# Kernel tuning notes

Hardware: AMD Instinct MI355X
Metric: run time of the kernel (lower is better)

The kernel has to match this reference:

```python
import jax, jax.numpy as jnp
import numpy as np

N = 50000   # nodes
E = 600000  # edges
D = 128     # in_size
H = 128     # hid_size
O = 10      # out_size


def setup_inputs() -> dict:
    key = jax.random.key(0)
    ks = jax.random.split(key, 11)
    features = jax.random.normal(ks[0], (N, D), dtype=jnp.float32)
    src = jax.random.randint(ks[1], (E,), 0, N, dtype=jnp.int32)
    dst = jax.random.randint(ks[2], (E,), 0, N, dtype=jnp.int32)
    s = 1.0 / np.sqrt(D)
    # 4 GraphConv layers: D->H, H->H, H->H, H->O (DGL GraphConv: weight + bias)
    W0 = jax.random.normal(ks[3], (D, H), jnp.float32) * s
    b0 = jnp.zeros((H,), jnp.float32)
    W1 = jax.random.normal(ks[4], (H, H), jnp.float32) * s
    b1 = jnp.zeros((H,), jnp.float32)
    W2 = jax.random.normal(ks[5], (H, H), jnp.float32) * s
    b2 = jnp.zeros((H,), jnp.float32)
    W3 = jax.random.normal(ks[6], (H, O), jnp.float32) * s
    b3 = jnp.zeros((O,), jnp.float32)
    return {"features": features, "src": src, "dst": dst,
            "W0": W0, "b0": b0, "W1": W1, "b1": b1,
            "W2": W2, "b2": b2, "W3": W3, "b3": b3}


def reference(features, src, dst, W0, b0, W1, b1, W2, b2, W3, b3):
    # DGL GraphConv with norm='both':
    #   h' = relu( D_in^{-1/2} A D_out^{-1/2} h W + b )
    # degrees clamped to >= 1; dropout is inference-mode identity.
    ones = jnp.ones((E,), features.dtype)
    out_deg = jax.ops.segment_sum(ones, src, num_segments=N)
    in_deg = jax.ops.segment_sum(ones, dst, num_segments=N)
    out_inv = jax.lax.rsqrt(jnp.maximum(out_deg, 1.0))[:, None]  # [N,1]
    in_inv = jax.lax.rsqrt(jnp.maximum(in_deg, 1.0))[:, None]    # [N,1]

    h = features
    layers = [(W0, b0, True), (W1, b1, True), (W2, b2, True), (W3, b3, False)]
    for W, b, act in layers:
        hs = h * out_inv                                   # src-side norm
        agg = jax.ops.segment_sum(hs[src], dst, num_segments=N)  # SpMM (copy_u + sum)
        h = (agg * in_inv) @ W + b                         # dst-side norm + linear
        if act:
            h = jax.nn.relu(h)
    return h
```

## Files before the change

### kernel.cpp

```cpp
#include <hip/hip_runtime.h>

#define NNODES 50000
#define NEDGES 600000
#define DH 128
#define SCAN_THREADS 512
#define SCAN_ELEMS 2048
#define SCAN_BLOCKS ((NNODES + SCAN_ELEMS - 1) / SCAN_ELEMS)
#define WCONV_BLOCKS ((3 * DH * DH) / 256)
#define NSLICES 32
#define NCHUNKS 8
#define CHUNK (NNODES / NCHUNKS)
#define ESLICE (NEDGES / NSLICES)
#define CNT_THREADS 1024

typedef __attribute__((ext_vector_type(4))) float f32x4;
typedef __attribute__((ext_vector_type(4))) _Float16 half4;
typedef __attribute__((ext_vector_type(8))) _Float16 half8;

__global__ __launch_bounds__(CNT_THREADS) void count_chunked(
        const int* __restrict__ src, const int* __restrict__ dst,
        int* __restrict__ partIn, int* __restrict__ partOut) {
    __shared__ int hin[CHUNK];
    __shared__ int hout[CHUNK];
    int slice = blockIdx.x >> 3;
    int chunk = blockIdx.x & 7;
    int cbase = chunk * CHUNK;
    int t = threadIdx.x;
    for (int i = t; i < CHUNK; i += CNT_THREADS) { hin[i] = 0; hout[i] = 0; }
    __syncthreads();
    int e0 = slice * ESLICE;
    int e1 = e0 + ESLICE;
    for (int e = e0 + t; e < e1; e += CNT_THREADS) {
        int d = dst[e];
        unsigned dd = (unsigned)(d - cbase);
        if (dd < CHUNK) atomicAdd(&hin[dd], 1);
        int s = src[e];
        unsigned ss = (unsigned)(s - cbase);
        if (ss < CHUNK) atomicAdd(&hout[ss], 1);
    }
    __syncthreads();
    int* pi = partIn  + slice * NNODES + cbase;
    int* po = partOut + slice * NNODES + cbase;
    for (int i = t; i < CHUNK; i += CNT_THREADS) { pi[i] = hin[i]; po[i] = hout[i]; }
}

__global__ void reduce_counts(const int* __restrict__ partIn, const int* __restrict__ partOut,
                              int* __restrict__ cnt_in, int* __restrict__ cnt_out, int N) {
    int n = blockIdx.x * blockDim.x + threadIdx.x;
    if (n >= N) return;
    int ti = 0, to = 0;
#pragma unroll
    for (int s = 0; s < NSLICES; ++s) {
        ti += partIn[s * NNODES + n];
        to += partOut[s * NNODES + n];
    }
    cnt_in[n] = ti;
    cnt_out[n] = to;
}

__global__ __launch_bounds__(SCAN_THREADS) void scan_sums(
        const int* __restrict__ counts, int* __restrict__ bsums, int N) {
    __shared__ int red[SCAN_THREADS / 64];
    int b = blockIdx.x, t = threadIdx.x;
    int base = b * SCAN_ELEMS + t * 4;
    int s = 0;
    if (base + 3 < N) {
        int4 v = *(const int4*)(counts + base);
        s = v.x + v.y + v.z + v.w;
    } else {
        for (int j = 0; j < 4; ++j) if (base + j < N) s += counts[base + j];
    }
#pragma unroll
    for (int off = 32; off > 0; off >>= 1) s += __shfl_down(s, off);
    if ((t & 63) == 0) red[t >> 6] = s;
    __syncthreads();
    if (t == 0) {
        int tot = 0;
#pragma unroll
        for (int w = 0; w < SCAN_THREADS / 64; ++w) tot += red[w];
        bsums[b] = tot;
    }
}

__global__ __launch_bounds__(SCAN_THREADS) void scan_final(
        const int* __restrict__ counts, const int* __restrict__ bsums,
        const int* __restrict__ cnt_out, int* __restrict__ off,
        int* __restrict__ cursor, float* __restrict__ out_inv,
        float* __restrict__ in_inv, int N, int nb) {
    __shared__ int lds[SCAN_THREADS];
    __shared__ int base_s;
    int b = blockIdx.x, t = threadIdx.x;
    if (t == 0) {
        int acc = 0;
        for (int i = 0; i < b; ++i) acc += bsums[i];
        base_s = acc;
    }
    int i0 = b * SCAN_ELEMS + t * 4;
    int v[4]; int s = 0;
#pragma unroll
    for (int j = 0; j < 4; ++j) {
        int idx = i0 + j;
        v[j] = (idx < N) ? counts[idx] : 0;
        s += v[j];
    }
    lds[t] = s;
    __syncthreads();
    for (int d = 1; d < SCAN_THREADS; d <<= 1) {
        int x = lds[t];
        int y = (t >= d) ? lds[t - d] : 0;
        __syncthreads();
        lds[t] = x + y;
        __syncthreads();
    }
    int excl = (t == 0) ? 0 : lds[t - 1];
    int run = base_s + excl;
#pragma unroll
    for (int j = 0; j < 4; ++j) {
        int idx = i0 + j;
        if (idx < N) {
            off[idx]    = run;
            cursor[idx] = run;
            in_inv[idx]  = rsqrtf(fmaxf((float)v[j], 1.0f));
            out_inv[idx] = rsqrtf(fmaxf((float)cnt_out[idx], 1.0f));
        }
        run += v[j];
    }
    if (b == nb - 1 && t == SCAN_THREADS - 1) off[N] = run;
}

__global__ void scatter_kernel(const int* __restrict__ src, const int* __restrict__ dst,
                               int* __restrict__ cursor, int* __restrict__ csr_src, int E) {
    int i = blockIdx.x * blockDim.x + threadIdx.x;
    if (i < E) {
        int pos = atomicAdd(&cursor[dst[i]], 1);
        csr_src[pos] = src[i];
    }
}

__global__ void prep_kernel(const float* __restrict__ W0, const float* __restrict__ W1,
                            const float* __restrict__ W2,
                            _Float16* __restrict__ WThi, _Float16* __restrict__ WTlo,
                            const float* __restrict__ fin, const float* __restrict__ out_inv,
                            _Float16* __restrict__ fout, int n4) {
    if (blockIdx.x < WCONV_BLOCKS) {
        int t = blockIdx.x * blockDim.x + threadIdx.x;
        int L = t >> 14;
        int idx = t & (DH * DH - 1);
        int n = idx >> 7;
        int k = idx & 127;
        const float* W = (L == 0) ? W0 : ((L == 1) ? W1 : W2);
        float w = W[k * DH + n];
        _Float16 hi = (_Float16)w;
        _Float16 lo = (_Float16)(w - (float)hi);
        WThi[t] = hi;
        WTlo[t] = lo;
    } else {
        int i = (blockIdx.x - WCONV_BLOCKS) * blockDim.x + threadIdx.x;
        if (i < n4) {
            float sc = out_inv[i >> 5];
            float4 v = ((const float4*)fin)[i];
            half4 h = {(_Float16)(v.x * sc), (_Float16)(v.y * sc),
                       (_Float16)(v.z * sc), (_Float16)(v.w * sc)};
            ((half4*)fout)[i] = h;
        }
    }
}

__global__ __launch_bounds__(256) void spmm_csr(
        const _Float16* __restrict__ h, const int* __restrict__ row_off,
        const int* __restrict__ csr_src,
        const float* __restrict__ in_inv, _Float16* __restrict__ X, int N) {
    int gw   = (blockIdx.x * blockDim.x + threadIdx.x) >> 6;
    int lane = threadIdx.x & 63;
    int half = lane >> 5;
    int l5   = lane & 31;
    int row  = gw * 2 + half;
    if (row >= N) return;
    int start = row_off[row], end = row_off[row + 1];
    float4 acc0 = make_float4(0.f, 0.f, 0.f, 0.f);
    float4 acc1 = make_float4(0.f, 0.f, 0.f, 0.f);
    int e = start;
    for (; e + 8 <= end; e += 8) {
        int s0 = csr_src[e];
        int s1 = csr_src[e + 1];
        int s2 = csr_src[e + 2];
        int s3 = csr_src[e + 3];
        int s4 = csr_src[e + 4];
        int s5 = csr_src[e + 5];
        int s6 = csr_src[e + 6];
        int s7 = csr_src[e + 7];
        half4 v0 = ((const half4*)(h + (size_t)s0 * DH))[l5];
        half4 v1 = ((const half4*)(h + (size_t)s1 * DH))[l5];
        half4 v2 = ((const half4*)(h + (size_t)s2 * DH))[l5];
        half4 v3 = ((const half4*)(h + (size_t)s3 * DH))[l5];
        half4 v4 = ((const half4*)(h + (size_t)s4 * DH))[l5];
        half4 v5 = ((const half4*)(h + (size_t)s5 * DH))[l5];
        half4 v6 = ((const half4*)(h + (size_t)s6 * DH))[l5];
        half4 v7 = ((const half4*)(h + (size_t)s7 * DH))[l5];
        acc0.x += (float)v0.x; acc0.y += (float)v0.y; acc0.z += (float)v0.z; acc0.w += (float)v0.w;
        acc1.x += (float)v1.x; acc1.y += (float)v1.y; acc1.z += (float)v1.z; acc1.w += (float)v1.w;
        acc0.x += (float)v2.x; acc0.y += (float)v2.y; acc0.z += (float)v2.z; acc0.w += (float)v2.w;
        acc1.x += (float)v3.x; acc1.y += (float)v3.y; acc1.z += (float)v3.z; acc1.w += (float)v3.w;
        acc0.x += (float)v4.x; acc0.y += (float)v4.y; acc0.z += (float)v4.z; acc0.w += (float)v4.w;
        acc1.x += (float)v5.x; acc1.y += (float)v5.y; acc1.z += (float)v5.z; acc1.w += (float)v5.w;
        acc0.x += (float)v6.x; acc0.y += (float)v6.y; acc0.z += (float)v6.z; acc0.w += (float)v6.w;
        acc1.x += (float)v7.x; acc1.y += (float)v7.y; acc1.z += (float)v7.z; acc1.w += (float)v7.w;
    }
    for (; e + 2 <= end; e += 2) {
        int s0 = csr_src[e];
        int s1 = csr_src[e + 1];
        half4 v0 = ((const half4*)(h + (size_t)s0 * DH))[l5];
        half4 v1 = ((const half4*)(h + (size_t)s1 * DH))[l5];
        acc0.x += (float)v0.x; acc0.y += (float)v0.y; acc0.z += (float)v0.z; acc0.w += (float)v0.w;
        acc1.x += (float)v1.x; acc1.y += (float)v1.y; acc1.z += (float)v1.z; acc1.w += (float)v1.w;
    }
    if (e < end) {
        int s0 = csr_src[e];
        half4 v0 = ((const half4*)(h + (size_t)s0 * DH))[l5];
        acc0.x += (float)v0.x; acc0.y += (float)v0.y; acc0.z += (float)v0.z; acc0.w += (float)v0.w;
    }
    float ii = in_inv[row];
    half4 o;
    o.x = (_Float16)((acc0.x + acc1.x) * ii);
    o.y = (_Float16)((acc0.y + acc1.y) * ii);
    o.z = (_Float16)((acc0.z + acc1.z) * ii);
    o.w = (_Float16)((acc0.w + acc1.w) * ii);
    ((half4*)(X + (size_t)row * DH))[l5] = o;
}

template<int RELU>
__global__ __launch_bounds__(256, 2) void gemm_mfma(
        const _Float16* __restrict__ X,
        const _Float16* __restrict__ WThi, const _Float16* __restrict__ WTlo,
        const float* __restrict__ bias, const float* __restrict__ out_inv,
        _Float16* __restrict__ Y, int Mtiles) {
    int lane  = threadIdx.x & 63;
    int gwave = (blockIdx.x * blockDim.x + threadIdx.x) >> 6;
    int nwav  = (gridDim.x * blockDim.x) >> 6;
    int nhalf = gwave & 1;
    int wstart  = gwave >> 1;
    int wstride = nwav >> 1;

    int r  = lane & 15;
    int kq = lane >> 4;

    half8 B[2][4][4];
#pragma unroll
    for (int nt = 0; nt < 4; ++nt) {
        int n = 64 * nhalf + 16 * nt + r;
#pragma unroll
        for (int kf = 0; kf < 4; ++kf) {
            B[0][nt][kf] = *(const half8*)(WThi + n * DH + 32 * kf + 8 * kq);
            B[1][nt][kf] = *(const half8*)(WTlo + n * DH + 32 * kf + 8 * kq);
        }
    }
    float bs[4];
#pragma unroll
    for (int nt = 0; nt < 4; ++nt) bs[nt] = bias[64 * nhalf + 16 * nt + r];

    for (int mt = wstart; mt < Mtiles; mt += wstride) {
        int m0 = mt * 16;
        const _Float16* xp = X + (size_t)(m0 + r) * DH + 8 * kq;
        half8 A[4];
#pragma unroll
        for (int kf = 0; kf < 4; ++kf)
            A[kf] = *(const half8*)(xp + 32 * kf);
        f32x4 acc[4];
#pragma unroll
        for (int nt = 0; nt < 4; ++nt)
            acc[nt] = (f32x4){bs[nt], bs[nt], bs[nt], bs[nt]};
#pragma unroll
        for (int kf = 0; kf < 4; ++kf) {
#pragma unroll
            for (int nt = 0; nt < 4; ++nt) {
                acc[nt] = __builtin_amdgcn_mfma_f32_16x16x32_f16(A[kf], B[0][nt][kf], acc[nt], 0, 0, 0);
                acc[nt] = __builtin_amdgcn_mfma_f32_16x16x32_f16(A[kf], B[1][nt][kf], acc[nt], 0, 0, 0);
            }
        }
        float sc[4];
#pragma unroll
        for (int j = 0; j < 4; ++j) sc[j] = out_inv[m0 + 4 * kq + j];
#pragma unroll
        for (int nt = 0; nt < 4; ++nt) {
            int n = 64 * nhalf + 16 * nt + r;
            _Float16* yp = Y + (size_t)(m0 + 4 * kq) * DH + n;
#pragma unroll
            for (int j = 0; j < 4; ++j) {
                float v = acc[nt][j];
                if (RELU) v = fmaxf(v, 0.f);
                yp[(size_t)j * DH] = (_Float16)(v * sc[j]);
            }
        }
    }
}

__global__ __launch_bounds__(256) void proj_out(
        const _Float16* __restrict__ X,
        const float* __restrict__ W, float* __restrict__ Z, int N) {
    __shared__ float Wl[DH * 10];
    for (int i = threadIdx.x; i < DH * 10; i += blockDim.x) Wl[i] = W[i];
    __syncthreads();

    int row = blockIdx.x * blockDim.x + threadIdx.x;
    if (row >= N) return;

    float acc[10];
#pragma unroll
    for (int o = 0; o < 10; ++o) acc[o] = 0.f;

    const half8* xp = (const half8*)(X + (size_t)row * DH);
#pragma unroll
    for (int q = 0; q < 16; ++q) {
        half8 v = xp[q];
#pragma unroll
        for (int j = 0; j < 8; ++j) {
            float x = (float)v[j];
            const float* wp = Wl + (q * 8 + j) * 10;
#pragma unroll
            for (int o = 0; o < 10; ++o)
                acc[o] += x * wp[o];
        }
    }
    float* zp = Z + (size_t)row * 10;
#pragma unroll
    for (int o = 0; o < 10; ++o) zp[o] = acc[o];
}

__global__ void agg10(const float* __restrict__ Z, const int* __restrict__ row_off,
                      const int* __restrict__ csr_src, const float* __restrict__ in_inv,
                      const float* __restrict__ b, float* __restrict__ out, int N) {
    int r = blockIdx.x * blockDim.x + threadIdx.x;
    if (r >= N) return;
    float2 acc[5] = {};
    int start = row_off[r], end = row_off[r + 1];
    for (int e = start; e < end; ++e) {
        int s = csr_src[e];
        const float2* zp = (const float2*)(Z + (size_t)s * 10);
#pragma unroll
        for (int o = 0; o < 5; ++o) {
            float2 z = zp[o];
            acc[o].x += z.x; acc[o].y += z.y;
        }
    }
    float ii = in_inv[r];
#pragma unroll
    for (int o = 0; o < 5; ++o) {
        out[(size_t)r * 10 + 2 * o]     = acc[o].x * ii + b[2 * o];
        out[(size_t)r * 10 + 2 * o + 1] = acc[o].y * ii + b[2 * o + 1];
    }
}

extern "C" void kernel_launch(void* const* d_in, const int* in_sizes, int n_in,
                              void* d_out, int out_size, void* d_ws, size_t ws_size,
                              hipStream_t stream) {
    const float* features = (const float*)d_in[0];
    const int*   src      = (const int*)d_in[1];
    const int*   dst      = (const int*)d_in[2];
    const float* W0 = (const float*)d_in[3];
    const float* b0 = (const float*)d_in[4];
    const float* W1 = (const float*)d_in[5];
    const float* b1 = (const float*)d_in[6];
    const float* W2 = (const float*)d_in[7];
    const float* b2 = (const float*)d_in[8];
    const float* W3 = (const float*)d_in[9];
    const float* b3 = (const float*)d_in[10];
    float* out = (float*)d_out;

    char* ws = (char*)d_ws;
    int*   cnt_out = (int*)ws;
    int*   cnt_in  = cnt_out + NNODES;
    int*   cursor  = cnt_in + NNODES;
    int*   row_off = cursor + NNODES;
    int*   bsums   = row_off + NNODES + 1;
    float* out_inv = (float*)(bsums + SCAN_BLOCKS);
    float* in_inv  = out_inv + NNODES;
    int*   csr_src = (int*)(in_inv + NNODES);
    size_t metaInts = (size_t)(6 * NNODES + 1 + SCAN_BLOCKS) + NEDGES;
    size_t off = ((metaInts * 4 + 255) / 256) * 256;
    _Float16* WThi = (_Float16*)(ws + off);  off += 3 * DH * DH * sizeof(_Float16);
    _Float16* WTlo = (_Float16*)(ws + off);  off += 3 * DH * DH * sizeof(_Float16);
    off = ((off + 255) / 256) * 256;
    _Float16* X16 = (_Float16*)(ws + off); off += (size_t)NNODES * DH * sizeof(_Float16);
    _Float16* Y16 = (_Float16*)(ws + off); off += (size_t)NNODES * DH * sizeof(_Float16);
    _Float16* F16 = (_Float16*)(ws + off); off += (size_t)NNODES * DH * sizeof(_Float16);
    float*  Z   = (float*)X16;
    int* partIn  = (int*)X16;
    int* partOut = (int*)Y16;

    const int n4 = NNODES * DH / 4;

    count_chunked<<<NSLICES * NCHUNKS, CNT_THREADS, 0, stream>>>(src, dst, partIn, partOut);
    reduce_counts<<<(NNODES + 255) / 256, 256, 0, stream>>>(partIn, partOut, cnt_in, cnt_out, NNODES);
    scan_sums<<<SCAN_BLOCKS, SCAN_THREADS, 0, stream>>>(cnt_in, bsums, NNODES);
    scan_final<<<SCAN_BLOCKS, SCAN_THREADS, 0, stream>>>(cnt_in, bsums, cnt_out, row_off,
                                                         cursor, out_inv, in_inv, NNODES, SCAN_BLOCKS);
    scatter_kernel<<<(NEDGES + 255) / 256, 256, 0, stream>>>(src, dst, cursor, csr_src, NEDGES);
    prep_kernel<<<WCONV_BLOCKS + (n4 + 255) / 256, 256, 0, stream>>>(W0, W1, W2, WThi, WTlo,
                                                                     features, out_inv, F16, n4);

    const int spmm_blocks = (NNODES / 2 + 3) / 4;
    const int Mtiles = NNODES / 16;
    const int gemm_blocks = 512;

    spmm_csr<<<spmm_blocks, 256, 0, stream>>>(F16, row_off, csr_src, in_inv, X16, NNODES);
    gemm_mfma<1><<<gemm_blocks, 256, 0, stream>>>(X16, WThi, WTlo, b0, out_inv, Y16, Mtiles);
    spmm_csr<<<spmm_blocks, 256, 0, stream>>>(Y16, row_off, csr_src, in_inv, X16, NNODES);
    gemm_mfma<1><<<gemm_blocks, 256, 0, stream>>>(X16, WThi + DH * DH, WTlo + DH * DH, b1, out_inv, Y16, Mtiles);
    spmm_csr<<<spmm_blocks, 256, 0, stream>>>(Y16, row_off, csr_src, in_inv, X16, NNODES);
    gemm_mfma<1><<<gemm_blocks, 256, 0, stream>>>(X16, WThi + 2 * DH * DH, WTlo + 2 * DH * DH, b2, out_inv, Y16, Mtiles);
    proj_out<<<(NNODES + 255) / 256, 256, 0, stream>>>(Y16, W3, Z, NNODES);
    agg10<<<(NNODES + 255) / 256, 256, 0, stream>>>(Z, row_off, csr_src, in_inv, b3, out, NNODES);
}
```

Measured before the change: 229.7 us.

## Fuse SpMM aggregation and MFMA GEMM into one per-tile layer kernel

Replaces the separate spmm_csr and gemm_mfma kernels with a single fused_layer kernel. Each 512-thread block aggregates 16 destination rows into an LDS tile, then eight waves each compute one 16-column slice of the tile with MFMA. This removes the fp16 intermediate X round-trip through global memory and two launches per layer. In exchange, every block reloads its weight fragments from global memory (3125 blocks instead of 512 persistent ones), and the gather phase now has a block-wide barrier before the GEMM, which can leave waves idle when row degrees are imbalanced.

```diff
diff --git a/kernel.cpp b/kernel.cpp
--- a/kernel.cpp
+++ b/kernel.cpp
@@ -12,6 +12,7 @@
 #define CHUNK (NNODES / NCHUNKS)
 #define ESLICE (NEDGES / NSLICES)
 #define CNT_THREADS 1024
+#define MTILES (NNODES / 16)
 
 typedef __attribute__((ext_vector_type(4))) float f32x4;
 typedef __attribute__((ext_vector_type(4))) _Float16 half4;
@@ -166,130 +167,106 @@
     }
 }
 
-__global__ __launch_bounds__(256) void spmm_csr(
+#define TP 136
+template<int RELU>
+__global__ __launch_bounds__(512) void fused_layer(
         const _Float16* __restrict__ h, const int* __restrict__ row_off,
-        const int* __restrict__ csr_src,
-        const float* __restrict__ in_inv, _Float16* __restrict__ X, int N) {
-    int gw   = (blockIdx.x * blockDim.x + threadIdx.x) >> 6;
-    int lane = threadIdx.x & 63;
+        const int* __restrict__ csr_src, const float* __restrict__ in_inv,
+        const _Float16* __restrict__ WThi, const _Float16* __restrict__ WTlo,
+        const float* __restrict__ bias, const float* __restrict__ out_inv,
+        _Float16* __restrict__ Y) {
+    __shared__ _Float16 tile[16][TP];
+    int tid  = threadIdx.x;
+    int wv   = tid >> 6;
+    int lane = tid & 63;
     int half = lane >> 5;
     int l5   = lane & 31;
-    int row  = gw * 2 + half;
-    if (row >= N) return;
-    int start = row_off[row], end = row_off[row + 1];
-    float4 acc0 = make_float4(0.f, 0.f, 0.f, 0.f);
-    float4 acc1 = make_float4(0.f, 0.f, 0.f, 0.f);
-    int e = start;
-    for (; e + 8 <= end; e += 8) {
-        int s0 = csr_src[e];
-        int s1 = csr_src[e + 1];
-        int s2 = csr_src[e + 2];
-        int s3 = csr_src[e + 3];
-        int s4 = csr_src[e + 4];
-        int s5 = csr_src[e + 5];
-        int s6 = csr_src[e + 6];
-        int s7 = csr_src[e + 7];
-        half4 v0 = ((const half4*)(h + (size_t)s0 * DH))[l5];
-        half4 v1 = ((const half4*)(h + (size_t)s1 * DH))[l5];
-        half4 v2 = ((const half4*)(h + (size_t)s2 * DH))[l5];
-        half4 v3 = ((const half4*)(h + (size_t)s3 * DH))[l5];
-        half4 v4 = ((const half4*)(h + (size_t)s4 * DH))[l5];
-        half4 v5 = ((const half4*)(h + (size_t)s5 * DH))[l5];
-        half4 v6 = ((const half4*)(h + (size_t)s6 * DH))[l5];
-        half4 v7 = ((const half4*)(h + (size_t)s7 * DH))[l5];
-        acc0.x += (float)v0.x; acc0.y += (float)v0.y; acc0.z += (float)v0.z; acc0.w += (float)v0.w;
-        acc1.x += (float)v1.x; acc1.y += (float)v1.y; acc1.z += (float)v1.z; acc1.w += (float)v1.w;
-        acc0.x += (float)v2.x; acc0.y += (float)v2.y; acc0.z += (float)v2.z; acc0.w += (float)v2.w;
-        acc1.x += (float)v3.x; acc1.y += (float)v3.y; acc1.z += (float)v3.z; acc1.w += (float)v3.w;
-        acc0.x += (float)v4.x; acc0.y += (float)v4.y; acc0.z += (float)v4.z; acc0.w += (float)v4.w;
-        acc1.x += (float)v5.x; acc1.y += (float)v5.y; acc1.z += (float)v5.z; acc1.w += (float)v5.w;
-        acc0.x += (float)v6.x; acc0.y += (float)v6.y; acc0.z += (float)v6.z; acc0.w += (float)v6.w;
-        acc1.x += (float)v7.x; acc1.y += (float)v7.y; acc1.z += (float)v7.z; acc1.w += (float)v7.w;
-    }
-    for (; e + 2 <= end; e += 2) {
-        int s0 = csr_src[e];
-        int s1 = csr_src[e + 1];
-        half4 v0 = ((const half4*)(h + (size_t)s0 * DH))[l5];
-        half4 v1 = ((const half4*)(h + (size_t)s1 * DH))[l5];
-        acc0.x += (float)v0.x; acc0.y += (float)v0.y; acc0.z += (float)v0.z; acc0.w += (float)v0.w;
-        acc1.x += (float)v1.x; acc1.y += (float)v1.y; acc1.z += (float)v1.z; acc1.w += (float)v1.w;
-    }
-    if (e < end) {
-        int s0 = csr_src[e];
-        half4 v0 = ((const half4*)(h + (size_t)s0 * DH))[l5];
-        acc0.x += (float)v0.x; acc0.y += (float)v0.y; acc0.z += (float)v0.z; acc0.w += (float)v0.w;
-    }
-    float ii = in_inv[row];
-    half4 o;
-    o.x = (_Float16)((acc0.x + acc1.x) * ii);
-    o.y = (_Float16)((acc0.y + acc1.y) * ii);
-    o.z = (_Float16)((acc0.z + acc1.z) * ii);
-    o.w = (_Float16)((acc0.w + acc1.w) * ii);
-    ((half4*)(X + (size_t)row * DH))[l5] = o;
-}
-
-template<int RELU>
-__global__ __launch_bounds__(256, 2) void gemm_mfma(
-        const _Float16* __restrict__ X,
-        const _Float16* __restrict__ WThi, const _Float16* __restrict__ WTlo,
-        const float* __restrict__ bias, const float* __restrict__ out_inv,
-        _Float16* __restrict__ Y, int Mtiles) {
-    int lane  = threadIdx.x & 63;
-    int gwave = (blockIdx.x * blockDim.x + threadIdx.x) >> 6;
-    int nwav  = (gridDim.x * blockDim.x) >> 6;
-    int nhalf = gwave & 1;
-    int wstart  = gwave >> 1;
-    int wstride = nwav >> 1;
-
-    int r  = lane & 15;
-    int kq = lane >> 4;
-
-    half8 B[2][4][4];
-#pragma unroll
-    for (int nt = 0; nt < 4; ++nt) {
-        int n = 64 * nhalf + 16 * nt + r;
+    int r    = lane & 15;
+    int kq   = lane >> 4;
+
+    int n = (wv << 4) + r;
+    half8 B0[4], B1[4];
+#pragma unroll
+    for (int kf = 0; kf < 4; ++kf) {
+        B0[kf] = *(const half8*)(WThi + n * DH + 32 * kf + 8 * kq);
+        B1[kf] = *(const half8*)(WTlo + n * DH + 32 * kf + 8 * kq);
+    }
+    float bs = bias[n];
+
+    int m0 = blockIdx.x << 4;
+
+    {
+        int row = m0 + (wv << 1) + half;
+        int start = row_off[row], end = row_off[row + 1];
+        float4 acc0 = make_float4(0.f, 0.f, 0.f, 0.f);
+        float4 acc1 = make_float4(0.f, 0.f, 0.f, 0.f);
+        int e = start;
+        for (; e + 8 <= end; e += 8) {
+            int s0 = csr_src[e];
+            int s1 = csr_src[e + 1];
+            int s2 = csr_src[e + 2];
+            int s3 = csr_src[e + 3];
+            int s4 = csr_src[e + 4];
+            int s5 = csr_src[e + 5];
+            int s6 = csr_src[e + 6];
+            int s7 = csr_src[e + 7];
+            half4 v0 = ((const half4*)(h + (size_t)s0 * DH))[l5];
+            half4 v1 = ((const half4*)(h + (size_t)s1 * DH))[l5];
+            half4 v2 = ((const half4*)(h + (size_t)s2 * DH))[l5];
+            half4 v3 = ((const half4*)(h + (size_t)s3 * DH))[l5];
+            half4 v4 = ((const half4*)(h + (size_t)s4 * DH))[l5];
+            half4 v5 = ((const half4*)(h + (size_t)s5 * DH))[l5];
+            half4 v6 = ((const half4*)(h + (size_t)s6 * DH))[l5];
+            half4 v7 = ((const half4*)(h + (size_t)s7 * DH))[l5];
+            acc0.x += (float)v0.x; acc0.y += (float)v0.y; acc0.z += (float)v0.z; acc0.w += (float)v0.w;
+            acc1.x += (float)v1.x; acc1.y += (float)v1.y; acc1.z += (float)v1.z; acc1.w += (float)v1.w;
+            acc0.x += (float)v2.x; acc0.y += (float)v2.y; acc0.z += (float)v2.z; acc0.w += (float)v2.w;
+            acc1.x += (float)v3.x; acc1.y += (float)v3.y; acc1.z += (float)v3.z; acc1.w += (float)v3.w;
+            acc0.x += (float)v4.x; acc0.y += (float)v4.y; acc0.z += (float)v4.z; acc0.w += (float)v4.w;
+            acc1.x += (float)v5.x; acc1.y += (float)v5.y; acc1.z += (float)v5.z; acc1.w += (float)v5.w;
+            acc0.x += (float)v6.x; acc0.y += (float)v6.y; acc0.z += (float)v6.z; acc0.w += (float)v6.w;
+            acc1.x += (float)v7.x; acc1.y += (float)v7.y; acc1.z += (float)v7.z; acc1.w += (float)v7.w;
+        }
+        for (; e + 2 <= end; e += 2) {
+            int s0 = csr_src[e];
+            int s1 = csr_src[e + 1];
+            half4 v0 = ((const half4*)(h + (size_t)s0 * DH))[l5];
+            half4 v1 = ((const half4*)(h + (size_t)s1 * DH))[l5];
+            acc0.x += (float)v0.x; acc0.y += (float)v0.y; acc0.z += (float)v0.z; acc0.w += (float)v0.w;
+            acc1.x += (float)v1.x; acc1.y += (float)v1.y; acc1.z += (float)v1.z; acc1.w += (float)v1.w;
+        }
+        if (e < end) {
+            int s0 = csr_src[e];
+            half4 v0 = ((const half4*)(h + (size_t)s0 * DH))[l5];
+            acc0.x += (float)v0.x; acc0.y += (float)v0.y; acc0.z += (float)v0.z; acc0.w += (float)v0.w;
+        }
+        float ii = in_inv[row];
+        half4 o;
+        o.x = (_Float16)((acc0.x + acc1.x) * ii);
+        o.y = (_Float16)((acc0.y + acc1.y) * ii);
+        o.z = (_Float16)((acc0.z + acc1.z) * ii);
+        o.w = (_Float16)((acc0.w + acc1.w) * ii);
+        *(half4*)(&tile[(wv << 1) + half][l5 * 4]) = o;
+    }
+    __syncthreads();
+
+    {
+        half8 A[4];
+#pragma unroll
+        for (int kf = 0; kf < 4; ++kf)
+            A[kf] = *(const half8*)(&tile[r][32 * kf + 8 * kq]);
+        f32x4 acc = (f32x4){bs, bs, bs, bs};
 #pragma unroll
         for (int kf = 0; kf < 4; ++kf) {
-            B[0][nt][kf] = *(const half8*)(WThi + n * DH + 32 * kf + 8 * kq);
-            B[1][nt][kf] = *(const half8*)(WTlo + n * DH + 32 * kf + 8 * kq);
-        }
-    }
-    float bs[4];
-#pragma unroll
-    for (int nt = 0; nt < 4; ++nt) bs[nt] = bias[64 * nhalf + 16 * nt + r];
-
-    for (int mt = wstart; mt < Mtiles; mt += wstride) {
-        int m0 = mt * 16;
-        const _Float16* xp = X + (size_t)(m0 + r) * DH + 8 * kq;
-        half8 A[4];
-#pragma unroll
-        for (int kf = 0; kf < 4; ++kf)
-            A[kf] = *(const half8*)(xp + 32 * kf);
-        f32x4 acc[4];
-#pragma unroll
-        for (int nt = 0; nt < 4; ++nt)
-            acc[nt] = (f32x4){bs[nt], bs[nt], bs[nt], bs[nt]};
-#pragma unroll
-        for (int kf = 0; kf < 4; ++kf) {
-#pragma unroll
-            for (int nt = 0; nt < 4; ++nt) {
-                acc[nt] = __builtin_amdgcn_mfma_f32_16x16x32_f16(A[kf], B[0][nt][kf], acc[nt], 0, 0, 0);
-                acc[nt] = __builtin_amdgcn_mfma_f32_16x16x32_f16(A[kf], B[1][nt][kf], acc[nt], 0, 0, 0);
-            }
-        }
-        float sc[4];
-#pragma unroll
-        for (int j = 0; j < 4; ++j) sc[j] = out_inv[m0 + 4 * kq + j];
-#pragma unroll
-        for (int nt = 0; nt < 4; ++nt) {
-            int n = 64 * nhalf + 16 * nt + r;
-            _Float16* yp = Y + (size_t)(m0 + 4 * kq) * DH + n;
-#pragma unroll
-            for (int j = 0; j < 4; ++j) {
-                float v = acc[nt][j];
-                if (RELU) v = fmaxf(v, 0.f);
-                yp[(size_t)j * DH] = (_Float16)(v * sc[j]);
-            }
+            acc = __builtin_amdgcn_mfma_f32_16x16x32_f16(A[kf], B0[kf], acc, 0, 0, 0);
+            acc = __builtin_amdgcn_mfma_f32_16x16x32_f16(A[kf], B1[kf], acc, 0, 0, 0);
+        }
+#pragma unroll
+        for (int j = 0; j < 4; ++j) {
+            float v = acc[j];
+            if (RELU) v = fmaxf(v, 0.f);
+            float sc = out_inv[m0 + 4 * kq + j];
+            Y[(size_t)(m0 + 4 * kq + j) * DH + n] = (_Float16)(v * sc);
         }
     }
 }
@@ -380,12 +357,12 @@
     _Float16* WThi = (_Float16*)(ws + off);  off += 3 * DH * DH * sizeof(_Float16);
     _Float16* WTlo = (_Float16*)(ws + off);  off += 3 * DH * DH * sizeof(_Float16);
     off = ((off + 255) / 256) * 256;
-    _Float16* X16 = (_Float16*)(ws + off); off += (size_t)NNODES * DH * sizeof(_Float16);
-    _Float16* Y16 = (_Float16*)(ws + off); off += (size_t)NNODES * DH * sizeof(_Float16);
+    _Float16* H1  = (_Float16*)(ws + off); off += (size_t)NNODES * DH * sizeof(_Float16);
+    _Float16* H2  = (_Float16*)(ws + off); off += (size_t)NNODES * DH * sizeof(_Float16);
     _Float16* F16 = (_Float16*)(ws + off); off += (size_t)NNODES * DH * sizeof(_Float16);
-    float*  Z   = (float*)X16;
-    int* partIn  = (int*)X16;
-    int* partOut = (int*)Y16;
+    float*  Z   = (float*)H2;
+    int* partIn  = (int*)H1;
+    int* partOut = (int*)H2;
 
     const int n4 = NNODES * DH / 4;
 
@@ -398,16 +375,12 @@
     prep_kernel<<<WCONV_BLOCKS + (n4 + 255) / 256, 256, 0, stream>>>(W0, W1, W2, WThi, WTlo,
                                                                      features, out_inv, F16, n4);
 
-    const int spmm_blocks = (NNODES / 2 + 3) / 4;
-    const int Mtiles = NNODES / 16;
-    const int gemm_blocks = 512;
-
-    spmm_csr<<<spmm_blocks, 256, 0, stream>>>(F16, row_off, csr_src, in_inv, X16, NNODES);
-    gemm_mfma<1><<<gemm_blocks, 256, 0, stream>>>(X16, WThi, WTlo, b0, out_inv, Y16, Mtiles);
-    spmm_csr<<<spmm_blocks, 256, 0, stream>>>(Y16, row_off, csr_src, in_inv, X16, NNODES);
-    gemm_mfma<1><<<gemm_blocks, 256, 0, stream>>>(X16, WThi + DH * DH, WTlo + DH * DH, b1, out_inv, Y16, Mtiles);
-    spmm_csr<<<spmm_blocks, 256, 0, stream>>>(Y16, row_off, csr_src, in_inv, X16, NNODES);
-    gemm_mfma<1><<<gemm_blocks, 256, 0, stream>>>(X16, WThi + 2 * DH * DH, WTlo + 2 * DH * DH, b2, out_inv, Y16, Mtiles);
-    proj_out<<<(NNODES + 255) / 256, 256, 0, stream>>>(Y16, W3, Z, NNODES);
+    fused_layer<1><<<MTILES, 512, 0, stream>>>(F16, row_off, csr_src, in_inv,
+                                               WThi, WTlo, b0, out_inv, H1);
+    fused_layer<1><<<MTILES, 512, 0, stream>>>(H1, row_off, csr_src, in_inv,
+                                               WThi + DH * DH, WTlo + DH * DH, b1, out_inv, H2);
+    fused_layer<1><<<MTILES, 512, 0, stream>>>(H2, row_off, csr_src, in_inv,
+                                               WThi + 2 * DH * DH, WTlo + 2 * DH * DH, b2, out_inv, H1);
+    proj_out<<<(NNODES + 255) / 256, 256, 0, stream>>>(H1, W3, Z, NNODES);
     agg10<<<(NNODES + 255) / 256, 256, 0, stream>>>(Z, row_off, csr_src, in_inv, b3, out, NNODES);
 }
```

New measurement: 270.4 us. 17.7% more time.
